# Kernel optimization log

Measured on AMD Instinct MI355X. Metric: run time of the kernel, lower is better.

## Reference

```python
import jax, jax.numpy as jnp
import numpy as np

N, E, G = 20000, 100000, 64          # nodes, edges, graphs in batch
IN, HID = 63, 128                    # in_feat, hidden_feat (per-head dim)
HEADS = (8, 8, 8)                    # num_heads per GATv2 layer
NCLS = 18
EPS = 1e-5


def setup_inputs() -> dict:
    key = jax.random.key(0)
    ks = list(jax.random.split(key, 48))
    it = iter(ks)
    nrm = lambda shape, s=0.05: jax.random.normal(next(it), shape, jnp.float32) * s

    inp = {
        "h": jax.random.normal(next(it), (N, IN), jnp.float32),
        "src": jax.random.randint(next(it), (E,), 0, N, dtype=jnp.int32),
        "dst": jax.random.randint(next(it), (E,), 0, N, dtype=jnp.int32),
        "gid": jnp.sort(jax.random.randint(next(it), (N,), 0, G, dtype=jnp.int32)),
    }
    dims = [(IN, HEADS[0] * HID), (HEADS[0] * HID, HEADS[1] * HID), (HEADS[1] * HID, HEADS[2] * HID)]
    for l, (din, dout) in enumerate(dims, 1):
        H = HEADS[l - 1]
        inp[f"w_src{l}"] = nrm((din, dout))
        inp[f"b_src{l}"] = jnp.zeros((dout,), jnp.float32)
        inp[f"w_dst{l}"] = nrm((din, dout))
        inp[f"b_dst{l}"] = jnp.zeros((dout,), jnp.float32)
        inp[f"attn{l}"] = nrm((H, HID))
        inp[f"bias{l}"] = jnp.zeros((dout,), jnp.float32)
        inp[f"gamma{l}"] = jnp.ones((dout,), jnp.float32)
        inp[f"beta{l}"] = jnp.zeros((dout,), jnp.float32)
    inp["fc1_w"] = nrm((HEADS[2] * HID, HID * 8))   # 1024 -> 1024 (hidden_feat*num_heads -> hidden_feat? see note)
    inp["fc1_b"] = jnp.zeros((HID * 8,), jnp.float32)
    inp["fc2_w"] = nrm((HID * 8, 1024))
    inp["fc2_b"] = jnp.zeros((1024,), jnp.float32)
    inp["fc3_w"] = nrm((1024, NCLS))
    inp["fc3_b"] = jnp.zeros((NCLS,), jnp.float32)
    return inp


def _gatv2(h, w_src, b_src, w_dst, b_dst, attn, bias, src, dst):
    """DGL GATv2Conv forward (dropouts are identity in eval mode)."""
    H, D = attn.shape
    fs = (h @ w_src + b_src).reshape(N, H, D)   # [N,H,D]
    fd = (h @ w_dst + b_dst).reshape(N, H, D)
    e = jax.nn.leaky_relu(fs[src] + fd[dst], 0.2)          # [E,H,D], GATv2 negative_slope=0.2
    sc = jnp.einsum('ehd,hd->eh', e, attn)                 # [E,H] attention logits
    m = jax.ops.segment_max(sc, dst, num_segments=N)       # segment-softmax over in-edges
    m = jnp.where(jnp.isfinite(m), m, 0.0)                 # guard isolated nodes
    ex = jnp.exp(sc - m[dst])
    den = jax.ops.segment_sum(ex, dst, num_segments=N)
    alpha = ex / den[dst]                                  # [E,H]
    out = jax.ops.segment_sum(alpha[..., None] * fs[src], dst, num_segments=N)  # [N,H,D]
    return out.reshape(N, H * D) + bias


def _bn(x, gamma, beta):
    mu = x.mean(0)
    var = x.var(0)  # biased, as torch BN uses for normalization
    return (x - mu) * jax.lax.rsqrt(var + EPS) * gamma + beta


def _lrelu(x):
    return jax.nn.leaky_relu(x, 0.01)  # torch F.leaky_relu default slope


def reference(h, src, dst, gid,
              w_src1, b_src1, w_dst1, b_dst1, attn1, bias1, gamma1, beta1,
              w_src2, b_src2, w_dst2, b_dst2, attn2, bias2, gamma2, beta2,
              w_src3, b_src3, w_dst3, b_dst3, attn3, bias3, gamma3, beta3,
              fc1_w, fc1_b, fc2_w, fc2_b, fc3_w, fc3_b):
    x = _lrelu(_bn(_gatv2(h, w_src1, b_src1, w_dst1, b_dst1, attn1, bias1, src, dst), gamma1, beta1))
    x = _lrelu(_bn(_gatv2(x, w_src2, b_src2, w_dst2, b_dst2, attn2, bias2, src, dst), gamma2, beta2))
    x = _lrelu(_bn(_gatv2(x, w_src3, b_src3, w_dst3, b_dst3, attn3, bias3, src, dst), gamma3, beta3))
    # AvgPooling: mean over nodes of each graph
    cnt = jax.ops.segment_sum(jnp.ones((N,), x.dtype), gid, num_segments=G)
    hg = jax.ops.segment_sum(x, gid, num_segments=G) / jnp.maximum(cnt, 1.0)[:, None]  # [G, 1024]
    z = _lrelu(hg @ fc1_w + fc1_b)
    z = _lrelu(z @ fc2_w + fc2_b)
    return z @ fc3_w + fc3_b  # [G, 18]
```

## Files before the change

### kernel.cpp

```cpp
#include <hip/hip_runtime.h>
#include <math.h>

#define N_NODES 20000
#define N_PAD   20096
#define N_EDGES 100000
#define N_GRAPHS 64
#define IN_F 63
#define NHEAD 8
#define F 1024
#define NCLS 18
#define BN_EPS 1e-5f
#define BN_CHUNKS 256

typedef __attribute__((ext_vector_type(8))) _Float16 half8v;
typedef __attribute__((ext_vector_type(4))) _Float16 half4v;
typedef __attribute__((ext_vector_type(4))) float f32x4;

__global__ void k_zero_i32(int* __restrict__ p, int n) {
    int i = blockIdx.x * blockDim.x + threadIdx.x;
    if (i < n) p[i] = 0;
}

__global__ void k_copy_i32(int* __restrict__ d, const int* __restrict__ s, int n) {
    int i = blockIdx.x * blockDim.x + threadIdx.x;
    if (i < n) d[i] = s[i];
}

__global__ void k_count(const int* __restrict__ dst, int* __restrict__ cnt) {
    int i = blockIdx.x * blockDim.x + threadIdx.x;
    if (i < N_EDGES) atomicAdd(&cnt[dst[i]], 1);
}

__global__ void k_scan(const int* __restrict__ cnt, int* __restrict__ off) {
    __shared__ int tsum[256];
    const int CH = (N_NODES + 255) / 256;
    int t = threadIdx.x;
    int s = 0;
    for (int i = 0; i < CH; ++i) {
        int idx = t * CH + i;
        if (idx < N_NODES) s += cnt[idx];
    }
    tsum[t] = s;
    __syncthreads();
    if (t == 0) {
        int acc = 0;
        for (int i = 0; i < 256; ++i) { int v = tsum[i]; tsum[i] = acc; acc += v; }
    }
    __syncthreads();
    int run = tsum[t];
    for (int i = 0; i < CH; ++i) {
        int idx = t * CH + i;
        if (idx < N_NODES) { off[idx] = run; run += cnt[idx]; }
    }
    if (t == 255) off[N_NODES] = run;
}

__global__ void k_fill(const int* __restrict__ dst, int* __restrict__ cursor,
                       int* __restrict__ csr_e) {
    int i = blockIdx.x * blockDim.x + threadIdx.x;
    if (i < N_EDGES) {
        int p = atomicAdd(&cursor[dst[i]], 1);
        csr_e[p] = i;
    }
}

__global__ void k_sort_buckets(const int* __restrict__ off, int* __restrict__ csr_e) {
    int n = blockIdx.x * blockDim.x + threadIdx.x;
    if (n >= N_NODES) return;
    int b = off[n], e = off[n + 1];
    for (int i = b + 1; i < e; ++i) {
        int v = csr_e[i];
        int j = i - 1;
        while (j >= b && csr_e[j] > v) { csr_e[j + 1] = csr_e[j]; --j; }
        csr_e[j + 1] = v;
    }
}

__global__ void k_gstart(const int* __restrict__ gid, int* __restrict__ gstart) {
    int g = blockIdx.x * blockDim.x + threadIdx.x;
    if (g > N_GRAPHS) return;
    int lo = 0, hi = N_NODES;
    while (lo < hi) {
        int mid = (lo + hi) >> 1;
        if (gid[mid] < g) lo = mid + 1; else hi = mid;
    }
    gstart[g] = lo;
}

__global__ void k_cvt_h(const float* __restrict__ h, _Float16* __restrict__ xh) {
    int idx = blockIdx.x * 256 + threadIdx.x;
    if (idx >= N_PAD * 64) return;
    int m = idx >> 6, k = idx & 63;
    float v = (m < N_NODES && k < IN_F) ? h[m * IN_F + k] : 0.f;
    xh[idx] = (_Float16)v;
}

__global__ void k_zero_pad(_Float16* __restrict__ xh) {
    int idx = blockIdx.x * 256 + threadIdx.x;
    const int total = (N_PAD - N_NODES) * F;
    if (idx < total) xh[(size_t)N_NODES * F + idx] = (_Float16)0.f;
}

__global__ void k_cvt_w2(const float* __restrict__ W0, _Float16* __restrict__ o0,
                         const float* __restrict__ W1, _Float16* __restrict__ o1,
                         int K, int Kpad) {
    const float* W = blockIdx.z ? W1 : W0;
    _Float16* wh = blockIdx.z ? o1 : o0;
    __shared__ float t[32][33];
    int kt = blockIdx.x * 32, nt = blockIdx.y * 32;
    int tx = threadIdx.x & 31, ty = threadIdx.x >> 5;
#pragma unroll
    for (int j = 0; j < 4; ++j) {
        int k = kt + ty + j * 8;
        t[ty + j * 8][tx] = (k < K) ? W[(size_t)k * F + nt + tx] : 0.f;
    }
    __syncthreads();
#pragma unroll
    for (int j = 0; j < 4; ++j) {
        int n = nt + ty + j * 8;
        wh[(size_t)n * Kpad + kt + tx] = (_Float16)t[tx][ty + j * 8];
    }
}

#define AS1C(p) ((const __attribute__((address_space(1))) void*)(p))
#define AS3(p)  ((__attribute__((address_space(3))) void*)(p))

__launch_bounds__(256, 2)
__global__ void k_gemm_dual(const _Float16* __restrict__ A,
                            const _Float16* __restrict__ Bs, const _Float16* __restrict__ Bd,
                            const float* __restrict__ bias_s, const float* __restrict__ bias_d,
                            _Float16* __restrict__ Cs, _Float16* __restrict__ Cd, int Kpad) {
    __shared__ _Float16 lds[2][2][128 * 64];
    const int l = threadIdx.x & 63, w = threadIdx.x >> 6;

    const int orig = blockIdx.y * 8 + blockIdx.x;
    const int wg = (orig & 7) * (N_PAD / 128) + (orig >> 3);
    const int by = wg >> 3, bx = wg & 7;

    const int grow = w * 32 + (l >> 3);
    const int gcol = ((l & 7) ^ (l >> 3)) << 3;
    const size_t rstep = (size_t)8 * Kpad;
    const _Float16* gBs = Bs + (size_t)(bx * 128 + grow) * Kpad + gcol;
    const _Float16* gBd = Bd + (size_t)(bx * 128 + grow) * Kpad + gcol;

    const int wr = (w >> 1) * 64, wc = (w & 1) * 64;
    const int frow = l & 15;
    const int swz = (l & 7) << 4;
    const int kbase = (l >> 4) * 16;

    const _Float16* pA = A + (size_t)(by * 128 + wr + frow) * Kpad + (l >> 4) * 8;

    f32x4 accS[4][4], accD[4][4];
    const f32x4 fzero = {0.f, 0.f, 0.f, 0.f};
#pragma unroll
    for (int i = 0; i < 4; ++i)
#pragma unroll
        for (int j = 0; j < 4; ++j) { accS[i][j] = fzero; accD[i][j] = fzero; }

    auto stage = [&](int b, int k0) {
        char* ds = (char*)&lds[b][0][0] + w * 4096;
        char* dd = (char*)&lds[b][1][0] + w * 4096;
#pragma unroll
        for (int j = 0; j < 4; ++j) {
            __builtin_amdgcn_global_load_lds(AS1C(gBs + k0 + j * rstep), AS3(ds + j * 1024), 16, 0, 0);
            __builtin_amdgcn_global_load_lds(AS1C(gBd + k0 + j * rstep), AS3(dd + j * 1024), 16, 0, 0);
        }
    };

    stage(0, 0);
    __syncthreads();

    int buf = 0;
    for (int k0 = 0; k0 < Kpad; k0 += 64) {
        half8v a[4][2];
#pragma unroll
        for (int mi = 0; mi < 4; ++mi)
#pragma unroll
            for (int kk = 0; kk < 2; ++kk)
                a[mi][kk] = *(const half8v*)(pA + (size_t)mi * 16 * Kpad + k0 + kk * 32);

        if (k0 + 64 < Kpad) stage(buf ^ 1, k0 + 64);

        const char* lbs = (const char*)&lds[buf][0][0];
        const char* lbd = (const char*)&lds[buf][1][0];
#pragma unroll
        for (int kk = 0; kk < 2; ++kk) {
            const int kb = (kk * 64 + kbase) ^ swz;
#pragma unroll
            for (int ni = 0; ni < 4; ++ni) {
                int rowb = wc + ni * 16 + frow;
                half8v bs = *(const half8v*)(lbs + rowb * 128 + kb);
                half8v bd = *(const half8v*)(lbd + rowb * 128 + kb);
#pragma unroll
                for (int mi = 0; mi < 4; ++mi) {
                    accS[mi][ni] = __builtin_amdgcn_mfma_f32_16x16x32_f16(a[mi][kk], bs, accS[mi][ni], 0, 0, 0);
                    accD[mi][ni] = __builtin_amdgcn_mfma_f32_16x16x32_f16(a[mi][kk], bd, accD[mi][ni], 0, 0, 0);
                }
            }
        }
        __syncthreads();
        buf ^= 1;
    }

    const int crow0 = by * 128 + wr + (l >> 4) * 4;
    const int ccol = bx * 128 + wc + (l & 15);
    float bS[4], bD[4];
#pragma unroll
    for (int ni = 0; ni < 4; ++ni) { bS[ni] = bias_s[ccol + ni * 16]; bD[ni] = bias_d[ccol + ni * 16]; }
#pragma unroll
    for (int mi = 0; mi < 4; ++mi) {
#pragma unroll
        for (int r = 0; r < 4; ++r) {
            int row = crow0 + mi * 16 + r;
            if (row < N_NODES) {
#pragma unroll
                for (int ni = 0; ni < 4; ++ni) {
                    int col = ccol + ni * 16;
                    Cs[(size_t)row * F + col] = (_Float16)(accS[mi][ni][r] + bS[ni]);
                    Cd[(size_t)row * F + col] = (_Float16)(accD[mi][ni][r] + bD[ni]);
                }
            }
        }
    }
}

__launch_bounds__(256)
__global__ void k_gat(const _Float16* __restrict__ fs, const _Float16* __restrict__ fd,
                      const int* __restrict__ off, const int* __restrict__ csr_e,
                      const int* __restrict__ src, const float* __restrict__ attn,
                      const float* __restrict__ bias, _Float16* __restrict__ y16) {
    __shared__ int s_src[256];
    const int n = blockIdx.x;
    const int t = threadIdx.x;
    const int b = off[n], e = off[n + 1];

    half4v fdv = *(const half4v*)(fd + (size_t)n * F + t * 4);
    const float fd0 = (float)fdv.x, fd1 = (float)fdv.y, fd2 = (float)fdv.z, fd3 = (float)fdv.w;
    const float4 av = *(const float4*)(attn + (t >> 5) * 128 + (t & 31) * 4);

    float m = -1e30f, den = 0.f;
    float ax = 0.f, ay = 0.f, az = 0.f, aw = 0.f;

    for (int c0 = b; c0 < e; c0 += 256) {
        int ncur = e - c0; if (ncur > 256) ncur = 256;
        __syncthreads();
        if (t < ncur) s_src[t] = src[csr_e[c0 + t]];
        __syncthreads();
        for (int i = 0; i < ncur; ++i) {
            int s = s_src[i];
            half4v fsv = *(const half4v*)(fs + (size_t)s * F + t * 4);
            float f0 = (float)fsv.x, f1 = (float)fsv.y, f2 = (float)fsv.z, f3 = (float)fsv.w;
            float vx = f0 + fd0; vx = vx > 0.f ? vx : 0.2f * vx;
            float vy = f1 + fd1; vy = vy > 0.f ? vy : 0.2f * vy;
            float vz = f2 + fd2; vz = vz > 0.f ? vz : 0.2f * vz;
            float vw = f3 + fd3; vw = vw > 0.f ? vw : 0.2f * vw;
            float p = vx * av.x + vy * av.y + vz * av.z + vw * av.w;
            p += __shfl_xor(p, 1);
            p += __shfl_xor(p, 2);
            p += __shfl_xor(p, 4);
            p += __shfl_xor(p, 8);
            p += __shfl_xor(p, 16);
            float mn = fmaxf(m, p);
            float so = __expf(m - mn);
            float wexp = __expf(p - mn);
            den = den * so + wexp;
            ax = ax * so + wexp * f0;
            ay = ay * so + wexp * f1;
            az = az * so + wexp * f2;
            aw = aw * so + wexp * f3;
            m = mn;
        }
    }
    float inv = (e > b) ? 1.f / den : 0.f;
    const float4 bb = *(const float4*)(bias + t * 4);
    half4v o;
    o.x = (_Float16)(ax * inv + bb.x);
    o.y = (_Float16)(ay * inv + bb.y);
    o.z = (_Float16)(az * inv + bb.z);
    o.w = (_Float16)(aw * inv + bb.w);
    *(half4v*)(y16 + (size_t)n * F + t * 4) = o;
}

__global__ void k_bnpart(const _Float16* __restrict__ y16, float* __restrict__ part) {
    const int ROWS = (N_NODES + BN_CHUNKS - 1) / BN_CHUNKS;
    int blk = blockIdx.x;
    int t = threadIdx.x;
    int r0 = blk * ROWS;
    int r1 = r0 + ROWS; if (r1 > N_NODES) r1 = N_NODES;
    float sx = 0.f, sy = 0.f, sz = 0.f, sw = 0.f;
    float qx = 0.f, qy = 0.f, qz = 0.f, qw = 0.f;
    for (int r = r0; r < r1; ++r) {
        half4v v = *(const half4v*)(y16 + (size_t)r * F + t * 4);
        float vx = (float)v.x, vy = (float)v.y, vz = (float)v.z, vw = (float)v.w;
        sx += vx; sy += vy; sz += vz; sw += vw;
        qx += vx * vx; qy += vy * vy; qz += vz * vz; qw += vw * vw;
    }
    float4 s4; s4.x = sx; s4.y = sy; s4.z = sz; s4.w = sw;
    float4 q4; q4.x = qx; q4.y = qy; q4.z = qz; q4.w = qw;
    *(float4*)(part + (size_t)blk * (2 * F) + t * 4) = s4;
    *(float4*)(part + (size_t)blk * (2 * F) + F + t * 4) = q4;
}

__global__ void k_bnfin(const float* __restrict__ part, const float* __restrict__ gamma,
                        const float* __restrict__ beta, float* __restrict__ scale,
                        float* __restrict__ shift) {
    int c = blockIdx.x * blockDim.x + threadIdx.x;
    if (c >= F) return;
    float s = 0.f, q = 0.f;
    for (int b = 0; b < BN_CHUNKS; ++b) {
        s += part[(size_t)b * (2 * F) + c];
        q += part[(size_t)b * (2 * F) + F + c];
    }
    float mu = s / (float)N_NODES;
    float var = q / (float)N_NODES - mu * mu;
    float sc = gamma[c] * rsqrtf(var + BN_EPS);
    scale[c] = sc;
    shift[c] = beta[c] - mu * sc;
}

__global__ void k_bnapply(const _Float16* __restrict__ y16, const float* __restrict__ scale,
                          const float* __restrict__ shift, float* __restrict__ x,
                          _Float16* __restrict__ xh, int mode) {
    int i = blockIdx.x * blockDim.x + threadIdx.x;
    if (i >= N_NODES * (F / 4)) return;
    int c4 = (i & (F / 4 - 1)) * 4;
    half4v v = ((const half4v*)y16)[i];
    float4 o;
    o.x = (float)v.x * scale[c4 + 0] + shift[c4 + 0];
    o.y = (float)v.y * scale[c4 + 1] + shift[c4 + 1];
    o.z = (float)v.z * scale[c4 + 2] + shift[c4 + 2];
    o.w = (float)v.w * scale[c4 + 3] + shift[c4 + 3];
    o.x = o.x > 0.f ? o.x : 0.01f * o.x;
    o.y = o.y > 0.f ? o.y : 0.01f * o.y;
    o.z = o.z > 0.f ? o.z : 0.01f * o.z;
    o.w = o.w > 0.f ? o.w : 0.01f * o.w;
    if (mode == 0) {
        half4v h4;
        h4.x = (_Float16)o.x; h4.y = (_Float16)o.y;
        h4.z = (_Float16)o.z; h4.w = (_Float16)o.w;
        *(half4v*)&xh[(size_t)i * 4] = h4;
    } else {
        ((float4*)x)[i] = o;
    }
}

__global__ void k_pool(const float* __restrict__ x, const int* __restrict__ gstart,
                       _Float16* __restrict__ hg16) {
    int g = blockIdx.y;
    int col = blockIdx.x * 256 + threadIdx.x;
    int r0 = gstart[g], r1 = gstart[g + 1];
    float s = 0.f;
    for (int r = r0; r < r1; ++r) s += x[(size_t)r * F + col];
    float inv = (r1 > r0) ? 1.f / (float)(r1 - r0) : 0.f;
    hg16[(size_t)g * F + col] = (_Float16)(s * inv);
}

__launch_bounds__(256)
__global__ void k_mlp_mfma(const _Float16* __restrict__ A16, const _Float16* __restrict__ Bt,
                           const float* __restrict__ bias, _Float16* __restrict__ out16,
                           float* __restrict__ out32, int mode) {
    const int l = threadIdx.x & 63, w = threadIdx.x >> 6;
    const int bx = blockIdx.x;
    const int fko = (l >> 4) * 8;

    const _Float16* pa = A16 + (size_t)(w * 16 + (l & 15)) * 1024 + fko;
    const _Float16* pb = Bt + (size_t)(bx * 64 + (l & 15)) * 1024 + fko;

    f32x4 acc[4];
    const f32x4 fzero = {0.f, 0.f, 0.f, 0.f};
#pragma unroll
    for (int ni = 0; ni < 4; ++ni) acc[ni] = fzero;

#pragma unroll 4
    for (int k0 = 0; k0 < 1024; k0 += 32) {
        half8v a = *(const half8v*)(pa + k0);
#pragma unroll
        for (int ni = 0; ni < 4; ++ni) {
            half8v b = *(const half8v*)(pb + (size_t)ni * 16 * 1024 + k0);
            acc[ni] = __builtin_amdgcn_mfma_f32_16x16x32_f16(a, b, acc[ni], 0, 0, 0);
        }
    }

    const int row0 = w * 16 + (l >> 4) * 4;
    const int col0 = bx * 64 + (l & 15);
#pragma unroll
    for (int ni = 0; ni < 4; ++ni) {
        int col = col0 + ni * 16;
        float bb = bias[col];
#pragma unroll
        for (int r = 0; r < 4; ++r) {
            float v = acc[ni][r] + bb;
            v = v > 0.f ? v : 0.01f * v;
            if (mode == 0) out16[(size_t)(row0 + r) * 1024 + col] = (_Float16)v;
            else out32[(size_t)(row0 + r) * 1024 + col] = v;
        }
    }
}

__global__ void k_fc3(const float* __restrict__ z2, const float* __restrict__ W,
                      const float* __restrict__ b, float* __restrict__ out) {
    int gw = (blockIdx.x * blockDim.x + threadIdx.x) >> 6;
    int lane = threadIdx.x & 63;
    if (gw >= N_GRAPHS * NCLS) return;
    int row = gw / NCLS, col = gw - row * NCLS;
    float s = 0.f;
    for (int k = lane; k < 1024; k += 64) s += z2[(size_t)row * 1024 + k] * W[(size_t)k * NCLS + col];
#pragma unroll
    for (int o = 32; o; o >>= 1) s += __shfl_down(s, o);
    if (lane == 0) out[(size_t)row * NCLS + col] = s + b[col];
}

extern "C" void kernel_launch(void* const* d_in, const int* in_sizes, int n_in,
                              void* d_out, int out_size, void* d_ws, size_t ws_size,
                              hipStream_t stream) {
    const float* h = (const float*)d_in[0];
    const int* src = (const int*)d_in[1];
    const int* dst = (const int*)d_in[2];
    const int* gid = (const int*)d_in[3];

    const float *w_src[3], *b_src[3], *w_dst[3], *b_dst[3], *attn[3], *bias[3], *gamma[3], *beta[3];
    for (int l = 0; l < 3; ++l) {
        int base = 4 + l * 8;
        w_src[l] = (const float*)d_in[base + 0];
        b_src[l] = (const float*)d_in[base + 1];
        w_dst[l] = (const float*)d_in[base + 2];
        b_dst[l] = (const float*)d_in[base + 3];
        attn[l]  = (const float*)d_in[base + 4];
        bias[l]  = (const float*)d_in[base + 5];
        gamma[l] = (const float*)d_in[base + 6];
        beta[l]  = (const float*)d_in[base + 7];
    }
    const float* fc1_w = (const float*)d_in[28];
    const float* fc1_b = (const float*)d_in[29];
    const float* fc2_w = (const float*)d_in[30];
    const float* fc2_b = (const float*)d_in[31];
    const float* fc3_w = (const float*)d_in[32];
    const float* fc3_b = (const float*)d_in[33];

    char* base = (char*)d_ws;
    size_t o = 0;
    auto carve = [&](size_t bytes) -> char* {
        char* p = base + o;
        o += (bytes + 255) & ~(size_t)255;
        return p;
    };
    _Float16* fs16 = (_Float16*)carve((size_t)N_NODES * F * 2);
    _Float16* fd16 = (_Float16*)carve((size_t)N_NODES * F * 2);
    _Float16* y16 = (_Float16*)carve((size_t)N_NODES * F * 2);
    float* x32 = (float*)carve((size_t)N_NODES * F * 4);
    _Float16* xh = (_Float16*)carve((size_t)N_PAD * F * 2);
    _Float16* wsh = (_Float16*)carve((size_t)F * F * 2);
    _Float16* wdh = (_Float16*)carve((size_t)F * F * 2);
    _Float16* fc1h = (_Float16*)carve((size_t)F * F * 2);
    _Float16* fc2h = (_Float16*)carve((size_t)F * F * 2);
    int* cnt = (int*)carve((size_t)N_NODES * 4);
    int* off = (int*)carve((size_t)(N_NODES + 1) * 4);
    int* cursor = (int*)carve((size_t)N_NODES * 4);
    int* csr_e = (int*)carve((size_t)N_EDGES * 4);
    float* part = (float*)carve((size_t)BN_CHUNKS * 2 * F * 4);
    float* scale = (float*)carve(F * 4);
    float* shift = (float*)carve(F * 4);
    int* gstart = (int*)carve((N_GRAPHS + 1) * 4);
    _Float16* hg16 = (_Float16*)carve((size_t)N_GRAPHS * F * 2);
    _Float16* z1h = (_Float16*)carve((size_t)N_GRAPHS * F * 2);
    float* z2 = (float*)carve((size_t)N_GRAPHS * F * 4);
    (void)ws_size;

    k_zero_i32<<<(N_NODES + 255) / 256, 256, 0, stream>>>(cnt, N_NODES);
    k_count<<<(N_EDGES + 255) / 256, 256, 0, stream>>>(dst, cnt);
    k_scan<<<1, 256, 0, stream>>>(cnt, off);
    k_copy_i32<<<(N_NODES + 255) / 256, 256, 0, stream>>>(cursor, off, N_NODES);
    k_fill<<<(N_EDGES + 255) / 256, 256, 0, stream>>>(dst, cursor, csr_e);
    k_sort_buckets<<<(N_NODES + 255) / 256, 256, 0, stream>>>(off, csr_e);
    k_gstart<<<1, 128, 0, stream>>>(gid, gstart);

    k_cvt_h<<<(N_PAD * 64 + 255) / 256, 256, 0, stream>>>(h, xh);
    k_zero_pad<<<((N_PAD - N_NODES) * F + 255) / 256, 256, 0, stream>>>(xh);
    k_cvt_w2<<<dim3(F / 32, F / 32, 2), 256, 0, stream>>>(fc1_w, fc1h, fc2_w, fc2h, F, F);

    const dim3 ggrid(8, N_PAD / 128);
    for (int l = 0; l < 3; ++l) {
        const int K = (l == 0) ? IN_F : F;
        const int Kp = (l == 0) ? 64 : F;
        k_cvt_w2<<<dim3(Kp / 32, F / 32, 2), 256, 0, stream>>>(w_src[l], wsh, w_dst[l], wdh, K, Kp);
        k_gemm_dual<<<ggrid, 256, 0, stream>>>(xh, wsh, wdh, b_src[l], b_dst[l], fs16, fd16, Kp);
        k_gat<<<N_NODES, 256, 0, stream>>>(fs16, fd16, off, csr_e, src, attn[l], bias[l], y16);
        k_bnpart<<<BN_CHUNKS, 256, 0, stream>>>(y16, part);
        k_bnfin<<<F / 256, 256, 0, stream>>>(part, gamma[l], beta[l], scale, shift);
        k_bnapply<<<(N_NODES * (F / 4) + 255) / 256, 256, 0, stream>>>(
            y16, scale, shift, x32, xh, (l == 2) ? 1 : 0);
    }

    k_pool<<<dim3(4, N_GRAPHS), 256, 0, stream>>>(x32, gstart, hg16);
    k_mlp_mfma<<<16, 256, 0, stream>>>(hg16, fc1h, fc1_b, z1h, nullptr, 0);
    k_mlp_mfma<<<16, 256, 0, stream>>>(z1h, fc2h, fc2_b, nullptr, z2, 1);
    k_fc3<<<(N_GRAPHS * NCLS * 64 + 255) / 256, 256, 0, stream>>>(z2, fc3_w, fc3_b, (float*)d_out);
}
```

Baseline: 880.2 us.

## Replace dual-output GEMM with single 128x128 tile GEMM over concatenated weights

The dual GEMM, which loaded A fragments directly from global memory and shared them across two weight matrices, is replaced by a conventional 128x128-tile GEMM. Both A and B are staged into LDS with async global_load_lds, and the src and dst weights are concatenated into one 2048-column matrix. This halves accumulator registers so occupancy can rise (launch bounds 2 to 4) and removes the uncoalesced direct global A loads. In exchange A is re-read twice as often across the doubled grid. K is now a template parameter and the grid swizzle is adjusted for 16 column tiles.

```diff
diff --git a/kernel.cpp b/kernel.cpp
--- a/kernel.cpp
+++ b/kernel.cpp
@@ -125,45 +125,43 @@
 #define AS1C(p) ((const __attribute__((address_space(1))) void*)(p))
 #define AS3(p)  ((__attribute__((address_space(3))) void*)(p))
 
-__launch_bounds__(256, 2)
-__global__ void k_gemm_dual(const _Float16* __restrict__ A,
-                            const _Float16* __restrict__ Bs, const _Float16* __restrict__ Bd,
-                            const float* __restrict__ bias_s, const float* __restrict__ bias_d,
-                            _Float16* __restrict__ Cs, _Float16* __restrict__ Cd, int Kpad) {
+template <int KPAD>
+__launch_bounds__(256, 4)
+__global__ void k_gemm(const _Float16* __restrict__ A, const _Float16* __restrict__ W,
+                       const float* __restrict__ bias_s, const float* __restrict__ bias_d,
+                       _Float16* __restrict__ Cs, _Float16* __restrict__ Cd) {
     __shared__ _Float16 lds[2][2][128 * 64];
     const int l = threadIdx.x & 63, w = threadIdx.x >> 6;
 
-    const int orig = blockIdx.y * 8 + blockIdx.x;
-    const int wg = (orig & 7) * (N_PAD / 128) + (orig >> 3);
-    const int by = wg >> 3, bx = wg & 7;
+    const int orig = blockIdx.y * 16 + blockIdx.x;
+    const int wg = (orig & 7) * (2512 / 8) + (orig >> 3);
+    const int by = wg >> 4, bx = wg & 15;
 
     const int grow = w * 32 + (l >> 3);
     const int gcol = ((l & 7) ^ (l >> 3)) << 3;
-    const size_t rstep = (size_t)8 * Kpad;
-    const _Float16* gBs = Bs + (size_t)(bx * 128 + grow) * Kpad + gcol;
-    const _Float16* gBd = Bd + (size_t)(bx * 128 + grow) * Kpad + gcol;
+    const size_t rstep = (size_t)8 * KPAD;
+    const _Float16* gA = A + (size_t)(by * 128 + grow) * KPAD + gcol;
+    const _Float16* gB = W + (size_t)(bx * 128 + grow) * KPAD + gcol;
 
     const int wr = (w >> 1) * 64, wc = (w & 1) * 64;
     const int frow = l & 15;
     const int swz = (l & 7) << 4;
     const int kbase = (l >> 4) * 16;
 
-    const _Float16* pA = A + (size_t)(by * 128 + wr + frow) * Kpad + (l >> 4) * 8;
-
-    f32x4 accS[4][4], accD[4][4];
+    f32x4 acc[4][4];
     const f32x4 fzero = {0.f, 0.f, 0.f, 0.f};
 #pragma unroll
     for (int i = 0; i < 4; ++i)
 #pragma unroll
-        for (int j = 0; j < 4; ++j) { accS[i][j] = fzero; accD[i][j] = fzero; }
+        for (int j = 0; j < 4; ++j) acc[i][j] = fzero;
 
     auto stage = [&](int b, int k0) {
-        char* ds = (char*)&lds[b][0][0] + w * 4096;
-        char* dd = (char*)&lds[b][1][0] + w * 4096;
+        char* dA = (char*)&lds[b][0][0] + w * 4096;
+        char* dB = (char*)&lds[b][1][0] + w * 4096;
 #pragma unroll
         for (int j = 0; j < 4; ++j) {
-            __builtin_amdgcn_global_load_lds(AS1C(gBs + k0 + j * rstep), AS3(ds + j * 1024), 16, 0, 0);
-            __builtin_amdgcn_global_load_lds(AS1C(gBd + k0 + j * rstep), AS3(dd + j * 1024), 16, 0, 0);
+            __builtin_amdgcn_global_load_lds(AS1C(gA + k0 + j * rstep), AS3(dA + j * 1024), 16, 0, 0);
+            __builtin_amdgcn_global_load_lds(AS1C(gB + k0 + j * rstep), AS3(dB + j * 1024), 16, 0, 0);
         }
     };
 
@@ -171,42 +169,42 @@
     __syncthreads();
 
     int buf = 0;
-    for (int k0 = 0; k0 < Kpad; k0 += 64) {
-        half8v a[4][2];
-#pragma unroll
-        for (int mi = 0; mi < 4; ++mi)
-#pragma unroll
-            for (int kk = 0; kk < 2; ++kk)
-                a[mi][kk] = *(const half8v*)(pA + (size_t)mi * 16 * Kpad + k0 + kk * 32);
-
-        if (k0 + 64 < Kpad) stage(buf ^ 1, k0 + 64);
-
-        const char* lbs = (const char*)&lds[buf][0][0];
-        const char* lbd = (const char*)&lds[buf][1][0];
+#pragma unroll 1
+    for (int k0 = 0; k0 < KPAD; k0 += 64) {
+        if (k0 + 64 < KPAD) stage(buf ^ 1, k0 + 64);
+
+        const char* lA = (const char*)&lds[buf][0][0];
+        const char* lB = (const char*)&lds[buf][1][0];
 #pragma unroll
         for (int kk = 0; kk < 2; ++kk) {
             const int kb = (kk * 64 + kbase) ^ swz;
+            half8v a[4];
+#pragma unroll
+            for (int mi = 0; mi < 4; ++mi) {
+                int row = wr + mi * 16 + frow;
+                a[mi] = *(const half8v*)(lA + row * 128 + kb);
+            }
 #pragma unroll
             for (int ni = 0; ni < 4; ++ni) {
                 int rowb = wc + ni * 16 + frow;
-                half8v bs = *(const half8v*)(lbs + rowb * 128 + kb);
-                half8v bd = *(const half8v*)(lbd + rowb * 128 + kb);
-#pragma unroll
-                for (int mi = 0; mi < 4; ++mi) {
-                    accS[mi][ni] = __builtin_amdgcn_mfma_f32_16x16x32_f16(a[mi][kk], bs, accS[mi][ni], 0, 0, 0);
-                    accD[mi][ni] = __builtin_amdgcn_mfma_f32_16x16x32_f16(a[mi][kk], bd, accD[mi][ni], 0, 0, 0);
-                }
+                half8v b = *(const half8v*)(lB + rowb * 128 + kb);
+#pragma unroll
+                for (int mi = 0; mi < 4; ++mi)
+                    acc[mi][ni] = __builtin_amdgcn_mfma_f32_16x16x32_f16(a[mi], b, acc[mi][ni], 0, 0, 0);
             }
         }
         __syncthreads();
         buf ^= 1;
     }
 
+    const bool isS = bx < 8;
+    _Float16* __restrict__ C = isS ? Cs : Cd;
+    const float* __restrict__ bias = isS ? bias_s : bias_d;
     const int crow0 = by * 128 + wr + (l >> 4) * 4;
-    const int ccol = bx * 128 + wc + (l & 15);
-    float bS[4], bD[4];
-#pragma unroll
-    for (int ni = 0; ni < 4; ++ni) { bS[ni] = bias_s[ccol + ni * 16]; bD[ni] = bias_d[ccol + ni * 16]; }
+    const int ccol = (bx & 7) * 128 + wc + (l & 15);
+    float bb[4];
+#pragma unroll
+    for (int ni = 0; ni < 4; ++ni) bb[ni] = bias[ccol + ni * 16];
 #pragma unroll
     for (int mi = 0; mi < 4; ++mi) {
 #pragma unroll
@@ -214,11 +212,8 @@
             int row = crow0 + mi * 16 + r;
             if (row < N_NODES) {
 #pragma unroll
-                for (int ni = 0; ni < 4; ++ni) {
-                    int col = ccol + ni * 16;
-                    Cs[(size_t)row * F + col] = (_Float16)(accS[mi][ni][r] + bS[ni]);
-                    Cd[(size_t)row * F + col] = (_Float16)(accD[mi][ni][r] + bD[ni]);
-                }
+                for (int ni = 0; ni < 4; ++ni)
+                    C[(size_t)row * F + ccol + ni * 16] = (_Float16)(acc[mi][ni][r] + bb[ni]);
             }
         }
     }
@@ -449,8 +444,7 @@
     _Float16* y16 = (_Float16*)carve((size_t)N_NODES * F * 2);
     float* x32 = (float*)carve((size_t)N_NODES * F * 4);
     _Float16* xh = (_Float16*)carve((size_t)N_PAD * F * 2);
-    _Float16* wsh = (_Float16*)carve((size_t)F * F * 2);
-    _Float16* wdh = (_Float16*)carve((size_t)F * F * 2);
+    _Float16* wcat = (_Float16*)carve((size_t)2 * F * F * 2);
     _Float16* fc1h = (_Float16*)carve((size_t)F * F * 2);
     _Float16* fc2h = (_Float16*)carve((size_t)F * F * 2);
     int* cnt = (int*)carve((size_t)N_NODES * 4);
@@ -478,12 +472,16 @@
     k_zero_pad<<<((N_PAD - N_NODES) * F + 255) / 256, 256, 0, stream>>>(xh);
     k_cvt_w2<<<dim3(F / 32, F / 32, 2), 256, 0, stream>>>(fc1_w, fc1h, fc2_w, fc2h, F, F);
 
-    const dim3 ggrid(8, N_PAD / 128);
+    const dim3 ggrid(16, N_PAD / 128);
     for (int l = 0; l < 3; ++l) {
         const int K = (l == 0) ? IN_F : F;
         const int Kp = (l == 0) ? 64 : F;
-        k_cvt_w2<<<dim3(Kp / 32, F / 32, 2), 256, 0, stream>>>(w_src[l], wsh, w_dst[l], wdh, K, Kp);
-        k_gemm_dual<<<ggrid, 256, 0, stream>>>(xh, wsh, wdh, b_src[l], b_dst[l], fs16, fd16, Kp);
+        k_cvt_w2<<<dim3(Kp / 32, F / 32, 2), 256, 0, stream>>>(
+            w_src[l], wcat, w_dst[l], wcat + (size_t)F * Kp, K, Kp);
+        if (Kp == 64)
+            k_gemm<64><<<ggrid, 256, 0, stream>>>(xh, wcat, b_src[l], b_dst[l], fs16, fd16);
+        else
+            k_gemm<1024><<<ggrid, 256, 0, stream>>>(xh, wcat, b_src[l], b_dst[l], fs16, fd16);
         k_gat<<<N_NODES, 256, 0, stream>>>(fs16, fd16, off, csr_e, src, attn[l], bias[l], y16);
         k_bnpart<<<BN_CHUNKS, 256, 0, stream>>>(y16, part);
         k_bnfin<<<F / 256, 256, 0, stream>>>(part, gamma[l], beta[l], scale, shift);
```

Measured after the change: 863.8 us. Within noise of the previous version (-1.9%).

## Stage A through LDS with triple-buffered GEMM pipeline and widen GAT per-thread vectors

Applied to the files above, without the earlier changes.

The dual GEMM now loads the A tile into LDS alongside both B tiles using async global-to-LDS copies with an XOR swizzle. It runs a three-stage ring buffer with K-step 32, explicit vmcnt waits and a single barrier per step, and the K dimension is a template parameter. The GAT aggregation kernel uses 128 threads per node, each handling 8 halfs, with one fewer shuffle step in the head reduction. Together these aim to hide memory latency in the GEMM and cut per-edge instruction overhead in GAT. The cost is more LDS use per block and fewer threads in flight per node.

```diff
diff --git a/kernel.cpp b/kernel.cpp
--- a/kernel.cpp
+++ b/kernel.cpp
@@ -125,30 +125,29 @@
 #define AS1C(p) ((const __attribute__((address_space(1))) void*)(p))
 #define AS3(p)  ((__attribute__((address_space(3))) void*)(p))
 
+template <int KPAD>
 __launch_bounds__(256, 2)
 __global__ void k_gemm_dual(const _Float16* __restrict__ A,
                             const _Float16* __restrict__ Bs, const _Float16* __restrict__ Bd,
                             const float* __restrict__ bias_s, const float* __restrict__ bias_d,
-                            _Float16* __restrict__ Cs, _Float16* __restrict__ Cd, int Kpad) {
-    __shared__ _Float16 lds[2][2][128 * 64];
+                            _Float16* __restrict__ Cs, _Float16* __restrict__ Cd) {
+    __shared__ _Float16 lds[3][3][128 * 32];
     const int l = threadIdx.x & 63, w = threadIdx.x >> 6;
 
     const int orig = blockIdx.y * 8 + blockIdx.x;
     const int wg = (orig & 7) * (N_PAD / 128) + (orig >> 3);
     const int by = wg >> 3, bx = wg & 7;
 
-    const int grow = w * 32 + (l >> 3);
-    const int gcol = ((l & 7) ^ (l >> 3)) << 3;
-    const size_t rstep = (size_t)8 * Kpad;
-    const _Float16* gBs = Bs + (size_t)(bx * 128 + grow) * Kpad + gcol;
-    const _Float16* gBd = Bd + (size_t)(bx * 128 + grow) * Kpad + gcol;
+    const int srow = w * 16 + (l >> 2);
+    const int schunk = ((l & 3) ^ ((l >> 2) & 3) ^ ((l >> 4) & 3)) << 3;
+    const _Float16* gA  = A  + (size_t)(by * 128 + srow) * KPAD + schunk;
+    const _Float16* gBs = Bs + (size_t)(bx * 128 + srow) * KPAD + schunk;
+    const _Float16* gBd = Bd + (size_t)(bx * 128 + srow) * KPAD + schunk;
+    const size_t jstep = (size_t)64 * KPAD;
 
     const int wr = (w >> 1) * 64, wc = (w & 1) * 64;
     const int frow = l & 15;
-    const int swz = (l & 7) << 4;
-    const int kbase = (l >> 4) * 16;
-
-    const _Float16* pA = A + (size_t)(by * 128 + wr + frow) * Kpad + (l >> 4) * 8;
+    const int kbyte = ((l & 3) ^ ((l >> 2) & 3) ^ ((l >> 4) & 3)) << 4;
 
     f32x4 accS[4][4], accD[4][4];
     const f32x4 fzero = {0.f, 0.f, 0.f, 0.f};
@@ -157,49 +156,51 @@
 #pragma unroll
         for (int j = 0; j < 4; ++j) { accS[i][j] = fzero; accD[i][j] = fzero; }
 
-    auto stage = [&](int b, int k0) {
-        char* ds = (char*)&lds[b][0][0] + w * 4096;
-        char* dd = (char*)&lds[b][1][0] + w * 4096;
-#pragma unroll
-        for (int j = 0; j < 4; ++j) {
-            __builtin_amdgcn_global_load_lds(AS1C(gBs + k0 + j * rstep), AS3(ds + j * 1024), 16, 0, 0);
-            __builtin_amdgcn_global_load_lds(AS1C(gBd + k0 + j * rstep), AS3(dd + j * 1024), 16, 0, 0);
+    auto stage = [&](int b, int t) {
+        const int k0 = t * 32;
+        char* dA  = (char*)&lds[b][0][0] + w * 1024;
+        char* dBs = (char*)&lds[b][1][0] + w * 1024;
+        char* dBd = (char*)&lds[b][2][0] + w * 1024;
+#pragma unroll
+        for (int j = 0; j < 2; ++j) {
+            __builtin_amdgcn_global_load_lds(AS1C(gA  + k0 + j * jstep), AS3(dA  + j * 4096), 16, 0, 0);
+            __builtin_amdgcn_global_load_lds(AS1C(gBs + k0 + j * jstep), AS3(dBs + j * 4096), 16, 0, 0);
+            __builtin_amdgcn_global_load_lds(AS1C(gBd + k0 + j * jstep), AS3(dBd + j * 4096), 16, 0, 0);
         }
     };
 
-    stage(0, 0);
-    __syncthreads();
-
-    int buf = 0;
-    for (int k0 = 0; k0 < Kpad; k0 += 64) {
-        half8v a[4][2];
+    auto compute = [&](int b) {
+        const char* lA  = (const char*)&lds[b][0][0];
+        const char* lBs = (const char*)&lds[b][1][0];
+        const char* lBd = (const char*)&lds[b][2][0];
+        half8v a[4];
 #pragma unroll
         for (int mi = 0; mi < 4; ++mi)
-#pragma unroll
-            for (int kk = 0; kk < 2; ++kk)
-                a[mi][kk] = *(const half8v*)(pA + (size_t)mi * 16 * Kpad + k0 + kk * 32);
-
-        if (k0 + 64 < Kpad) stage(buf ^ 1, k0 + 64);
-
-        const char* lbs = (const char*)&lds[buf][0][0];
-        const char* lbd = (const char*)&lds[buf][1][0];
-#pragma unroll
-        for (int kk = 0; kk < 2; ++kk) {
-            const int kb = (kk * 64 + kbase) ^ swz;
-#pragma unroll
-            for (int ni = 0; ni < 4; ++ni) {
-                int rowb = wc + ni * 16 + frow;
-                half8v bs = *(const half8v*)(lbs + rowb * 128 + kb);
-                half8v bd = *(const half8v*)(lbd + rowb * 128 + kb);
-#pragma unroll
-                for (int mi = 0; mi < 4; ++mi) {
-                    accS[mi][ni] = __builtin_amdgcn_mfma_f32_16x16x32_f16(a[mi][kk], bs, accS[mi][ni], 0, 0, 0);
-                    accD[mi][ni] = __builtin_amdgcn_mfma_f32_16x16x32_f16(a[mi][kk], bd, accD[mi][ni], 0, 0, 0);
-                }
+            a[mi] = *(const half8v*)(lA + (wr + mi * 16 + frow) * 64 + kbyte);
+#pragma unroll
+        for (int ni = 0; ni < 4; ++ni) {
+            const int rb = (wc + ni * 16 + frow) * 64 + kbyte;
+            half8v bs = *(const half8v*)(lBs + rb);
+            half8v bd = *(const half8v*)(lBd + rb);
+#pragma unroll
+            for (int mi = 0; mi < 4; ++mi) {
+                accS[mi][ni] = __builtin_amdgcn_mfma_f32_16x16x32_f16(a[mi], bs, accS[mi][ni], 0, 0, 0);
+                accD[mi][ni] = __builtin_amdgcn_mfma_f32_16x16x32_f16(a[mi], bd, accD[mi][ni], 0, 0, 0);
             }
         }
-        __syncthreads();
-        buf ^= 1;
+    };
+
+    constexpr int NT = KPAD / 32;
+    stage(0, 0);
+    if (NT > 1) stage(1, 1);
+#pragma unroll 1
+    for (int t = 0; t < NT; ++t) {
+        if (t == NT - 1) asm volatile("s_waitcnt vmcnt(0)" ::: "memory");
+        else             asm volatile("s_waitcnt vmcnt(6)" ::: "memory");
+        __builtin_amdgcn_s_barrier();
+        __builtin_amdgcn_sched_barrier(0);
+        if (t + 2 < NT) stage((t + 2) % 3, t + 2);
+        compute(t % 3);
     }
 
     const int crow0 = by * 128 + wr + (l >> 4) * 4;
@@ -224,61 +225,66 @@
     }
 }
 
-__launch_bounds__(256)
+__launch_bounds__(128)
 __global__ void k_gat(const _Float16* __restrict__ fs, const _Float16* __restrict__ fd,
                       const int* __restrict__ off, const int* __restrict__ csr_e,
                       const int* __restrict__ src, const float* __restrict__ attn,
                       const float* __restrict__ bias, _Float16* __restrict__ y16) {
-    __shared__ int s_src[256];
+    __shared__ int s_src[128];
     const int n = blockIdx.x;
     const int t = threadIdx.x;
     const int b = off[n], e = off[n + 1];
 
-    half4v fdv = *(const half4v*)(fd + (size_t)n * F + t * 4);
-    const float fd0 = (float)fdv.x, fd1 = (float)fdv.y, fd2 = (float)fdv.z, fd3 = (float)fdv.w;
-    const float4 av = *(const float4*)(attn + (t >> 5) * 128 + (t & 31) * 4);
+    half8v fdv8 = *(const half8v*)(fd + (size_t)n * F + t * 8);
+    float fdv[8], av[8];
+    const float4 a0 = *(const float4*)(attn + (t >> 4) * 128 + (t & 15) * 8);
+    const float4 a1 = *(const float4*)(attn + (t >> 4) * 128 + (t & 15) * 8 + 4);
+    av[0] = a0.x; av[1] = a0.y; av[2] = a0.z; av[3] = a0.w;
+    av[4] = a1.x; av[5] = a1.y; av[6] = a1.z; av[7] = a1.w;
+#pragma unroll
+    for (int j = 0; j < 8; ++j) fdv[j] = (float)fdv8[j];
 
     float m = -1e30f, den = 0.f;
-    float ax = 0.f, ay = 0.f, az = 0.f, aw = 0.f;
-
-    for (int c0 = b; c0 < e; c0 += 256) {
-        int ncur = e - c0; if (ncur > 256) ncur = 256;
+    float acc[8] = {0.f, 0.f, 0.f, 0.f, 0.f, 0.f, 0.f, 0.f};
+
+    for (int c0 = b; c0 < e; c0 += 128) {
+        int ncur = e - c0; if (ncur > 128) ncur = 128;
         __syncthreads();
         if (t < ncur) s_src[t] = src[csr_e[c0 + t]];
         __syncthreads();
         for (int i = 0; i < ncur; ++i) {
             int s = s_src[i];
-            half4v fsv = *(const half4v*)(fs + (size_t)s * F + t * 4);
-            float f0 = (float)fsv.x, f1 = (float)fsv.y, f2 = (float)fsv.z, f3 = (float)fsv.w;
-            float vx = f0 + fd0; vx = vx > 0.f ? vx : 0.2f * vx;
-            float vy = f1 + fd1; vy = vy > 0.f ? vy : 0.2f * vy;
-            float vz = f2 + fd2; vz = vz > 0.f ? vz : 0.2f * vz;
-            float vw = f3 + fd3; vw = vw > 0.f ? vw : 0.2f * vw;
-            float p = vx * av.x + vy * av.y + vz * av.z + vw * av.w;
+            half8v fsv8 = *(const half8v*)(fs + (size_t)s * F + t * 8);
+            float f[8];
+            float p = 0.f;
+#pragma unroll
+            for (int j = 0; j < 8; ++j) {
+                f[j] = (float)fsv8[j];
+                float v = f[j] + fdv[j];
+                v = v > 0.f ? v : 0.2f * v;
+                p += v * av[j];
+            }
             p += __shfl_xor(p, 1);
             p += __shfl_xor(p, 2);
             p += __shfl_xor(p, 4);
             p += __shfl_xor(p, 8);
-            p += __shfl_xor(p, 16);
             float mn = fmaxf(m, p);
             float so = __expf(m - mn);
             float wexp = __expf(p - mn);
             den = den * so + wexp;
-            ax = ax * so + wexp * f0;
-            ay = ay * so + wexp * f1;
-            az = az * so + wexp * f2;
-            aw = aw * so + wexp * f3;
+#pragma unroll
+            for (int j = 0; j < 8; ++j) acc[j] = acc[j] * so + wexp * f[j];
             m = mn;
         }
     }
     float inv = (e > b) ? 1.f / den : 0.f;
-    const float4 bb = *(const float4*)(bias + t * 4);
-    half4v o;
-    o.x = (_Float16)(ax * inv + bb.x);
-    o.y = (_Float16)(ay * inv + bb.y);
-    o.z = (_Float16)(az * inv + bb.z);
-    o.w = (_Float16)(aw * inv + bb.w);
-    *(half4v*)(y16 + (size_t)n * F + t * 4) = o;
+    const float4 b0 = *(const float4*)(bias + t * 8);
+    const float4 b1 = *(const float4*)(bias + t * 8 + 4);
+    float bb[8] = {b0.x, b0.y, b0.z, b0.w, b1.x, b1.y, b1.z, b1.w};
+    half8v o;
+#pragma unroll
+    for (int j = 0; j < 8; ++j) o[j] = (_Float16)(acc[j] * inv + bb[j]);
+    *(half8v*)(y16 + (size_t)n * F + t * 8) = o;
 }
 
 __global__ void k_bnpart(const _Float16* __restrict__ y16, float* __restrict__ part) {
@@ -483,8 +489,11 @@
         const int K = (l == 0) ? IN_F : F;
         const int Kp = (l == 0) ? 64 : F;
         k_cvt_w2<<<dim3(Kp / 32, F / 32, 2), 256, 0, stream>>>(w_src[l], wsh, w_dst[l], wdh, K, Kp);
-        k_gemm_dual<<<ggrid, 256, 0, stream>>>(xh, wsh, wdh, b_src[l], b_dst[l], fs16, fd16, Kp);
-        k_gat<<<N_NODES, 256, 0, stream>>>(fs16, fd16, off, csr_e, src, attn[l], bias[l], y16);
+        if (Kp == 64)
+            k_gemm_dual<64><<<ggrid, 256, 0, stream>>>(xh, wsh, wdh, b_src[l], b_dst[l], fs16, fd16);
+        else
+            k_gemm_dual<1024><<<ggrid, 256, 0, stream>>>(xh, wsh, wdh, b_src[l], b_dst[l], fs16, fd16);
+        k_gat<<<N_NODES, 128, 0, stream>>>(fs16, fd16, off, csr_e, src, attn[l], bias[l], y16);
         k_bnpart<<<BN_CHUNKS, 256, 0, stream>>>(y16, part);
         k_bnfin<<<F / 256, 256, 0, stream>>>(part, gamma[l], beta[l], scale, shift);
         k_bnapply<<<(N_NODES * (F / 4) + 255) / 256, 256, 0, stream>>>(
```

After: 793.2 us. -9.9%, faster.
